# Performance work log

Hardware: AMD Instinct MI355X
Metric: run time of the kernel (lower is better)

The kernel has to match this reference:

```python
import jax, jax.numpy as jnp
import numpy as np

N, C, H, W = 16, 80, 200, 152
STRIDE = 8
PRE_NMS_THRESH = 0.2
K = 100            # pre_nms_top_n (== fpn_post_nms_top_n)
NMS_THRESH = 0.6
MIN_SIZE = 0.0


def setup_inputs() -> dict:
    key = jax.random.key(0)
    k1, k2, k3 = jax.random.split(key, 3)
    # shift logits down so only a realistic fraction passes sigmoid > 0.2
    box_cls = jax.random.normal(k1, (N, C, H, W), jnp.float32) - 2.0
    box_regression = jax.random.uniform(k2, (N, 4, H, W), jnp.float32) * 64.0
    centerness = jax.random.normal(k3, (N, 1, H, W), jnp.float32)
    ys, xs = jnp.meshgrid(jnp.arange(H), jnp.arange(W), indexing='ij')
    locations = jnp.stack([xs * STRIDE + STRIDE // 2,
                           ys * STRIDE + STRIDE // 2], axis=-1)
    locations = locations.reshape(-1, 2).astype(jnp.float32)  # [HW, 2] (x, y)
    return {"locations": locations, "box_cls": box_cls,
            "box_regression": box_regression, "centerness": centerness,
            "size_h": H * STRIDE, "size_w": W * STRIDE}


def _iou_matrix(boxes):
    # boxes: [K, 4] xyxy -> pairwise IoU [K, K]
    area = jnp.clip(boxes[:, 2] - boxes[:, 0], 0) * jnp.clip(boxes[:, 3] - boxes[:, 1], 0)
    lt = jnp.maximum(boxes[:, None, :2], boxes[None, :, :2])
    rb = jnp.minimum(boxes[:, None, 2:], boxes[None, :, 2:])
    wh = jnp.clip(rb - lt, 0)
    inter = wh[..., 0] * wh[..., 1]
    return inter / (area[:, None] + area[None, :] - inter + 1e-9)


def _nms_keep(iou, valid):
    # boxes assumed sorted by score (desc). Sequential greedy suppression.
    k = valid.shape[0]
    ar = jnp.arange(k)
    def body(i, keep):
        suppressed = jnp.any(keep & (ar < i) & (iou[i] > NMS_THRESH))
        return keep.at[i].set(valid[i] & ~suppressed)
    return jax.lax.fori_loop(0, k, body, valid)


def reference(locations, box_cls, box_regression, centerness, size_h, size_w):
    n, c = box_cls.shape[0], box_cls.shape[1]
    # N,C,H,W -> N,HW,C ; sigmoid scores
    scores = jax.nn.sigmoid(box_cls.transpose(0, 2, 3, 1).reshape(n, -1, c))
    reg = box_regression.transpose(0, 2, 3, 1).reshape(n, -1, 4)        # [n,HW,4]
    ctr = jax.nn.sigmoid(centerness.transpose(0, 2, 3, 1).reshape(n, -1))  # [n,HW]
    cand = scores > PRE_NMS_THRESH
    comb = scores * ctr[:, :, None]
    # masked flat scores; top-K == topk(per_pre_nms_top_n) with -inf padding
    masked = jnp.where(cand, comb, -jnp.inf).reshape(n, -1)
    vals, idx = jax.lax.top_k(masked, K)          # sorted desc, [n,K]
    valid = jnp.isfinite(vals)
    loc_idx = idx // c                            # flat location index in HW
    labels = idx % c + 1
    per_reg = jnp.take_along_axis(reg, loc_idx[:, :, None], axis=1)  # [n,K,4]
    per_loc = locations[loc_idx]                                     # [n,K,2]
    x1 = per_loc[..., 0] - per_reg[..., 0]
    y1 = per_loc[..., 1] - per_reg[..., 1]
    x2 = per_loc[..., 0] + per_reg[..., 2]
    y2 = per_loc[..., 1] + per_reg[..., 3]
    wmax = jnp.float32(size_w - 1)
    hmax = jnp.float32(size_h - 1)
    x1 = jnp.clip(x1, 0, wmax); x2 = jnp.clip(x2, 0, wmax)
    y1 = jnp.clip(y1, 0, hmax); y2 = jnp.clip(y2, 0, hmax)
    boxes = jnp.stack([x1, y1, x2, y2], axis=-1)  # [n,K,4]
    valid = valid & (x2 - x1 >= MIN_SIZE) & (y2 - y1 >= MIN_SIZE)
    # scores = sqrt(cls * centerness); double-where keeps grads finite
    scores_out = jnp.where(valid, jnp.sqrt(jnp.where(valid, vals, 1.0)), 0.0)
    # multi-class NMS: offset boxes per class so classes never overlap
    off = labels.astype(boxes.dtype) * jnp.float32(max(size_h, size_w))
    boxes_off = boxes + off[..., None]
    iou = jax.vmap(_iou_matrix)(boxes_off)        # [n,K,K]
    keep = jax.vmap(_nms_keep)(iou, valid)        # [n,K] bool
    scores_final = jnp.where(keep, scores_out, 0.0)
    return boxes, scores_final, labels, keep
```

## Files before the change

kernel.cpp:

```cpp
#include <hip/hip_runtime.h>
#include <math.h>

#define NIMG 16
#define NC   80
#define HH   200
#define WW   152
#define HWSZ (HH*WW)
#define HW4  (HWSZ/4)
#define KTOP 100
#define NBINS 4096
#define CAP   16384
#define FCAP  1024
#define CHUNKS4 30
#define CHUNKS 119

#define HIST_OFF 0
#define CNT_OFF  262144
#define TBIN_OFF 262208
#define CIDX_OFF 262272
#define CVAL_OFF 1310848
#define ZERO_BYTES 262272

__device__ __forceinline__ float sigf(float x){ return 1.f/(1.f+expf(-x)); }

__global__ void __launch_bounds__(256) k_hist_collect(
    const float* __restrict__ cls, const float* __restrict__ cent,
    int* __restrict__ hist, int* __restrict__ cnt,
    int* __restrict__ cand_idx, float* __restrict__ cand_val)
{
  __shared__ int lhist[NBINS];
  __shared__ int lcnt, gbase;
  __shared__ int   lidx[FCAP];
  __shared__ float lval[FCAP];
  const int n    = blockIdx.y;
  const int idx4 = blockIdx.x*256 + threadIdx.x;
  for (int b = threadIdx.x; b < NBINS; b += 256) lhist[b] = 0;
  if (threadIdx.x == 0) lcnt = 0;
  __syncthreads();
  if (idx4 < HW4) {
    const float4 ct4 = ((const float4*)cent)[n*HW4 + idx4];
    float cs[4];
    cs[0] = sigf(ct4.x); cs[1] = sigf(ct4.y); cs[2] = sigf(ct4.z); cs[3] = sigf(ct4.w);
    const float4* cp = (const float4*)(cls + (size_t)n*NC*HWSZ) + idx4;
    const int hw0 = idx4*4;
    for (int c = 0; c < NC; ++c) {
      float4 v = cp[(size_t)c*HW4];
      float x[4] = {v.x, v.y, v.z, v.w};
      #pragma unroll
      for (int e = 0; e < 4; ++e) {
        if (x[e] > -1.3867f) {
          float s = sigf(x[e]);
          if (s > 0.2f) {
            float comb = s*cs[e];
            if (comb > 0.25f) {
              int b = (int)(comb*4096.f); if (b > 4095) b = 4095;
              atomicAdd(&lhist[b], 1);
              if (comb > 0.5f) {
                int p = atomicAdd(&lcnt, 1);
                if (p < FCAP) { lidx[p] = (hw0+e)*NC + c; lval[p] = comb; }
                else {
                  int g = atomicAdd(&cnt[n], 1);
                  if (g < CAP) { cand_idx[n*CAP+g] = (hw0+e)*NC + c; cand_val[n*CAP+g] = comb; }
                }
              }
            }
          }
        }
      }
    }
  }
  __syncthreads();
  int nc = lcnt; if (nc > FCAP) nc = FCAP;
  if (threadIdx.x == 0) gbase = atomicAdd(&cnt[n], nc);
  __syncthreads();
  for (int i = threadIdx.x; i < nc; i += 256) {
    int g = gbase + i;
    if (g < CAP) { cand_idx[n*CAP+g] = lidx[i]; cand_val[n*CAP+g] = lval[i]; }
  }
  for (int b = threadIdx.x; b < NBINS; b += 256) {
    int v = lhist[b];
    if (v) atomicAdd(&hist[n*NBINS + b], v);
  }
}

__global__ void __launch_bounds__(256) k_thresh(
    const int* __restrict__ hist, int* __restrict__ tbin)
{
  __shared__ int lh[NBINS];
  __shared__ int csum[256];
  const int n = blockIdx.x, t = threadIdx.x;
  for (int b = t; b < NBINS; b += 256) lh[b] = hist[n*NBINS + b];
  __syncthreads();
  int s = 0;
  for (int b = t*16; b < t*16+16; ++b) s += lh[b];
  csum[t] = s;
  __syncthreads();
  if (t == 0) { int run = 0; for (int i = 255; i >= 0; --i) { int tmp = csum[i]; csum[i] = run; run += tmp; } }
  __syncthreads();
  int run = csum[t];
  for (int b = t*16+15; b >= t*16; --b) {
    run += lh[b];
    if (run >= KTOP && (run - lh[b]) < KTOP) tbin[n] = b;
  }
}

__global__ void __launch_bounds__(256) k_collect_fb(
    const float* __restrict__ cls, const float* __restrict__ cent,
    const int* __restrict__ tbin, int* __restrict__ cnt,
    int* __restrict__ cand_idx, float* __restrict__ cand_val)
{
  const int n = blockIdx.y;
  const int T = tbin[n];
  if (T >= 2048) return;
  __shared__ int lcnt, gbase;
  __shared__ int   lidx[FCAP];
  __shared__ float lval[FCAP];
  if (threadIdx.x == 0) lcnt = 0;
  __syncthreads();
  const int hw = blockIdx.x*256 + threadIdx.x;
  if (hw < HWSZ) {
    float csv = sigf(cent[n*HWSZ + hw]);
    const float* cp = cls + (size_t)n*NC*HWSZ + hw;
    for (int c = 0; c < NC; ++c) {
      float s = sigf(cp[(size_t)c*HWSZ]);
      if (s > 0.2f) {
        float comb = s*csv;
        if (!(comb > 0.5f)) {
          int b = (int)(comb*4096.f); if (b > 4095) b = 4095;
          if (b >= T) {
            int p = atomicAdd(&lcnt, 1);
            if (p < FCAP) { lidx[p] = hw*NC + c; lval[p] = comb; }
            else { int g = atomicAdd(&cnt[n], 1);
                   if (g < CAP) { cand_idx[n*CAP+g] = hw*NC + c; cand_val[n*CAP+g] = comb; } }
          }
        }
      }
    }
  }
  __syncthreads();
  int ncl = lcnt; if (ncl > FCAP) ncl = FCAP;
  if (threadIdx.x == 0) gbase = atomicAdd(&cnt[n], ncl);
  __syncthreads();
  for (int i = threadIdx.x; i < ncl; i += 256) {
    int g = gbase + i;
    if (g < CAP) { cand_idx[n*CAP+g] = lidx[i]; cand_val[n*CAP+g] = lval[i]; }
  }
}

__global__ void __launch_bounds__(256) k_final(
    const float* __restrict__ cls, const float* __restrict__ cent,
    const float* __restrict__ reg, const float* __restrict__ locs,
    const int* __restrict__ tbin, const int* __restrict__ cnt,
    const int* __restrict__ cand_idx, const float* __restrict__ cand_val,
    float* __restrict__ out)
{
  const int n = blockIdx.x, tid = threadIdx.x;
  __shared__ int    fidx[FCAP];
  __shared__ double fval[FCAP];
  __shared__ int fcnt;
  __shared__ int    topidx[KTOP];
  __shared__ double topval[KTOP];
  __shared__ float bx1[KTOP], by1[KTOP], bx2[KTOP], by2[KTOP], barea[KTOP];
  __shared__ float ox1[KTOP], oy1[KTOP], ox2[KTOP], oy2[KTOP], osc[KTOP];
  __shared__ int olab[KTOP];
  __shared__ unsigned char oval[KTOP], okeep[KTOP];
  if (tid == 0) fcnt = 0;
  for (int k = tid; k < KTOP; k += 256) topidx[k] = -1;
  __syncthreads();
  const int T = tbin[n];
  int m = cnt[n]; if (m > CAP) m = CAP;
  for (int i = tid; i < m; i += 256) {
    float v = cand_val[n*CAP + i];
    int b = (int)(v*4096.f); if (b > 4095) b = 4095;
    if (b >= T) { int p = atomicAdd(&fcnt, 1); if (p < FCAP) fidx[p] = cand_idx[n*CAP + i]; }
  }
  __syncthreads();
  int mf = fcnt; if (mf > FCAP) mf = FCAP;
  for (int i = tid; i < mf; i += 256) {
    int idx = fidx[i]; int loc = idx / NC; int c = idx - loc*NC;
    double s  = 1.0/(1.0 + exp(-(double)cls[(size_t)n*NC*HWSZ + (size_t)c*HWSZ + loc]));
    double ct = 1.0/(1.0 + exp(-(double)cent[n*HWSZ + loc]));
    fval[i] = s*ct;
  }
  __syncthreads();
  for (int i = tid; i < mf; i += 256) {
    double vi = fval[i]; int ii = fidx[i]; int r = 0;
    for (int j = 0; j < mf; ++j) {
      double vj = fval[j];
      r += (vj > vi) || (vj == vi && fidx[j] < ii);
    }
    if (r < KTOP) { topidx[r] = ii; topval[r] = vi; }
  }
  __syncthreads();
  if (tid < KTOP) {
    int idx = topidx[tid];
    float x1, y1, x2, y2, sc; int lab; bool vld;
    if (idx >= 0) {
      int loc = idx / NC; int c = idx - loc*NC; lab = c + 1;
      float lx = locs[2*loc], ly = locs[2*loc + 1];
      const float* rp = reg + (size_t)n*4*HWSZ;
      float dl = rp[loc], dt = rp[HWSZ + loc], dr = rp[2*HWSZ + loc], db = rp[3*HWSZ + loc];
      const float wmax = (float)(WW*8 - 1);
      const float hmax = (float)(HH*8 - 1);
      x1 = fminf(fmaxf(lx - dl, 0.f), wmax);
      x2 = fminf(fmaxf(lx + dr, 0.f), wmax);
      y1 = fminf(fmaxf(ly - dt, 0.f), hmax);
      y2 = fminf(fmaxf(ly + db, 0.f), hmax);
      vld = (x2 - x1 >= 0.f) && (y2 - y1 >= 0.f);
      sc = vld ? sqrtf((float)topval[tid]) : 0.f;
    } else { x1 = y1 = x2 = y2 = 0.f; lab = 1; vld = false; sc = 0.f; }
    ox1[tid] = x1; oy1[tid] = y1; ox2[tid] = x2; oy2[tid] = y2;
    osc[tid] = sc; olab[tid] = lab; oval[tid] = vld ? 1 : 0;
    float off = (float)lab * 1600.0f;
    float X1 = x1 + off, Y1 = y1 + off, X2 = x2 + off, Y2 = y2 + off;
    bx1[tid] = X1; by1[tid] = Y1; bx2[tid] = X2; by2[tid] = Y2;
    barea[tid] = fmaxf(X2 - X1, 0.f) * fmaxf(Y2 - Y1, 0.f);
  }
  __syncthreads();
  if (tid < 64) {
    const int lane = tid, j1 = lane + 64;
    float a_x1 = bx1[lane], a_y1 = by1[lane], a_x2 = bx2[lane], a_y2 = by2[lane], a_ar = barea[lane];
    float c_x1 = 0, c_y1 = 0, c_x2 = 0, c_y2 = 0, c_ar = 0;
    if (j1 < KTOP) { c_x1 = bx1[j1]; c_y1 = by1[j1]; c_x2 = bx2[j1]; c_y2 = by2[j1]; c_ar = barea[j1]; }
    unsigned long long k0 = 0ull, k1 = 0ull;
    for (int i = 0; i < KTOP; ++i) {
      float ix1 = bx1[i], iy1 = by1[i], ix2 = bx2[i], iy2 = by2[i], iar = barea[i];
      bool s0 = false, s1 = false;
      if (lane < i && ((k0 >> lane) & 1ull)) {
        float w = fmaxf(fminf(ix2, a_x2) - fmaxf(ix1, a_x1), 0.f);
        float h = fmaxf(fminf(iy2, a_y2) - fmaxf(iy1, a_y1), 0.f);
        float inter = w*h;
        s0 = inter / (iar + a_ar - inter + 1e-9f) > 0.6f;
      }
      if (j1 < i && ((k1 >> lane) & 1ull)) {
        float w = fmaxf(fminf(ix2, c_x2) - fmaxf(ix1, c_x1), 0.f);
        float h = fmaxf(fminf(iy2, c_y2) - fmaxf(iy1, c_y1), 0.f);
        float inter = w*h;
        s1 = inter / (iar + c_ar - inter + 1e-9f) > 0.6f;
      }
      unsigned long long b0 = __ballot(s0), b1 = __ballot(s1);
      bool keep_i = (oval[i] != 0) && ((b0 | b1) == 0ull);
      if (keep_i) { if (i < 64) k0 |= 1ull << i; else k1 |= 1ull << (i - 64); }
    }
    okeep[lane] = (unsigned char)((k0 >> lane) & 1ull);
    if (j1 < KTOP) okeep[j1] = (unsigned char)((k1 >> lane) & 1ull);
  }
  __syncthreads();
  if (tid < KTOP) {
    float* ob = out;
    float* os = out + NIMG*KTOP*4;
    float* ol = os + NIMG*KTOP;
    float* ok = ol + NIMG*KTOP;
    int base = n*KTOP + tid;
    ob[base*4 + 0] = ox1[tid]; ob[base*4 + 1] = oy1[tid];
    ob[base*4 + 2] = ox2[tid]; ob[base*4 + 3] = oy2[tid];
    bool kp = okeep[tid] != 0;
    os[base] = kp ? osc[tid] : 0.f;
    ol[base] = (float)olab[tid];
    ok[base] = kp ? 1.f : 0.f;
  }
}

extern "C" void kernel_launch(void* const* d_in, const int* in_sizes, int n_in,
                              void* d_out, int out_size, void* d_ws, size_t ws_size,
                              hipStream_t stream) {
  const float* locs = (const float*)d_in[0];
  const float* cls  = (const float*)d_in[1];
  const float* reg  = (const float*)d_in[2];
  const float* cent = (const float*)d_in[3];
  char* ws = (char*)d_ws;
  int*   hist     = (int*)(ws + HIST_OFF);
  int*   cnt      = (int*)(ws + CNT_OFF);
  int*   tbin     = (int*)(ws + TBIN_OFF);
  int*   cand_idx = (int*)(ws + CIDX_OFF);
  float* cand_val = (float*)(ws + CVAL_OFF);
  float* out = (float*)d_out;

  hipMemsetAsync(d_ws, 0, ZERO_BYTES, stream);
  dim3 gridA(CHUNKS4, NIMG);
  k_hist_collect<<<gridA, 256, 0, stream>>>(cls, cent, hist, cnt, cand_idx, cand_val);
  k_thresh<<<NIMG, 256, 0, stream>>>(hist, tbin);
  dim3 gridF(CHUNKS, NIMG);
  k_collect_fb<<<gridF, 256, 0, stream>>>(cls, cent, tbin, cnt, cand_idx, cand_val);
  k_final<<<NIMG, 256, 0, stream>>>(cls, cent, reg, locs, tbin, cnt,
                                    cand_idx, cand_val, out);
}
```

Measured before the change: 336.2 us.

## Drop global histogram pass; split class loop across blocks and refine threshold in final

```diff
diff --git a/kernel.cpp b/kernel.cpp
--- a/kernel.cpp
+++ b/kernel.cpp
@@ -10,59 +10,53 @@
 #define KTOP 100
 #define NBINS 4096
 #define CAP   16384
+#define SCAP  512
 #define FCAP  1024
+#define CPG   16
+#define CGRP  (NC/CPG)
 #define CHUNKS4 30
-#define CHUNKS 119
-
-#define HIST_OFF 0
-#define CNT_OFF  262144
-#define TBIN_OFF 262208
-#define CIDX_OFF 262272
-#define CVAL_OFF 1310848
-#define ZERO_BYTES 262272
+
+#define CNT_OFF  0
+#define TBIN_OFF 64
+#define CIDX_OFF 128
+#define CVAL_OFF (128 + NIMG*CAP*4)
+#define ZERO_BYTES 128
 
 __device__ __forceinline__ float sigf(float x){ return 1.f/(1.f+expf(-x)); }
 
-__global__ void __launch_bounds__(256) k_hist_collect(
+__global__ void __launch_bounds__(256) k_collect(
     const float* __restrict__ cls, const float* __restrict__ cent,
-    int* __restrict__ hist, int* __restrict__ cnt,
-    int* __restrict__ cand_idx, float* __restrict__ cand_val)
+    int* __restrict__ cnt, int* __restrict__ cand_idx, float* __restrict__ cand_val)
 {
-  __shared__ int lhist[NBINS];
   __shared__ int lcnt, gbase;
-  __shared__ int   lidx[FCAP];
-  __shared__ float lval[FCAP];
-  const int n    = blockIdx.y;
+  __shared__ int   lidx[SCAP];
+  __shared__ float lval[SCAP];
+  const int n = blockIdx.y, g = blockIdx.z;
   const int idx4 = blockIdx.x*256 + threadIdx.x;
-  for (int b = threadIdx.x; b < NBINS; b += 256) lhist[b] = 0;
   if (threadIdx.x == 0) lcnt = 0;
   __syncthreads();
   if (idx4 < HW4) {
     const float4 ct4 = ((const float4*)cent)[n*HW4 + idx4];
     float cs[4];
     cs[0] = sigf(ct4.x); cs[1] = sigf(ct4.y); cs[2] = sigf(ct4.z); cs[3] = sigf(ct4.w);
-    const float4* cp = (const float4*)(cls + (size_t)n*NC*HWSZ) + idx4;
+    const float4* cp = (const float4*)(cls + (size_t)n*NC*HWSZ + (size_t)g*CPG*HWSZ) + idx4;
     const int hw0 = idx4*4;
-    for (int c = 0; c < NC; ++c) {
+    #pragma unroll 4
+    for (int c = 0; c < CPG; ++c) {
       float4 v = cp[(size_t)c*HW4];
       float x[4] = {v.x, v.y, v.z, v.w};
       #pragma unroll
       for (int e = 0; e < 4; ++e) {
-        if (x[e] > -1.3867f) {
+        if (x[e] > 0.f) {
           float s = sigf(x[e]);
-          if (s > 0.2f) {
-            float comb = s*cs[e];
-            if (comb > 0.25f) {
-              int b = (int)(comb*4096.f); if (b > 4095) b = 4095;
-              atomicAdd(&lhist[b], 1);
-              if (comb > 0.5f) {
-                int p = atomicAdd(&lcnt, 1);
-                if (p < FCAP) { lidx[p] = (hw0+e)*NC + c; lval[p] = comb; }
-                else {
-                  int g = atomicAdd(&cnt[n], 1);
-                  if (g < CAP) { cand_idx[n*CAP+g] = (hw0+e)*NC + c; cand_val[n*CAP+g] = comb; }
-                }
-              }
+          float comb = s*cs[e];
+          if (comb > 0.5f) {
+            int gi = (hw0+e)*NC + (g*CPG + c);
+            int p = atomicAdd(&lcnt, 1);
+            if (p < SCAP) { lidx[p] = gi; lval[p] = comb; }
+            else {
+              int gg = atomicAdd(&cnt[n], 1);
+              if (gg < CAP) { cand_idx[n*CAP+gg] = gi; cand_val[n*CAP+gg] = comb; }
             }
           }
         }
@@ -70,80 +64,62 @@
     }
   }
   __syncthreads();
-  int nc = lcnt; if (nc > FCAP) nc = FCAP;
+  int nc = lcnt; if (nc > SCAP) nc = SCAP;
   if (threadIdx.x == 0) gbase = atomicAdd(&cnt[n], nc);
   __syncthreads();
   for (int i = threadIdx.x; i < nc; i += 256) {
-    int g = gbase + i;
-    if (g < CAP) { cand_idx[n*CAP+g] = lidx[i]; cand_val[n*CAP+g] = lval[i]; }
-  }
-  for (int b = threadIdx.x; b < NBINS; b += 256) {
-    int v = lhist[b];
-    if (v) atomicAdd(&hist[n*NBINS + b], v);
-  }
-}
-
-__global__ void __launch_bounds__(256) k_thresh(
-    const int* __restrict__ hist, int* __restrict__ tbin)
-{
-  __shared__ int lh[NBINS];
-  __shared__ int csum[256];
-  const int n = blockIdx.x, t = threadIdx.x;
-  for (int b = t; b < NBINS; b += 256) lh[b] = hist[n*NBINS + b];
-  __syncthreads();
-  int s = 0;
-  for (int b = t*16; b < t*16+16; ++b) s += lh[b];
-  csum[t] = s;
-  __syncthreads();
-  if (t == 0) { int run = 0; for (int i = 255; i >= 0; --i) { int tmp = csum[i]; csum[i] = run; run += tmp; } }
-  __syncthreads();
-  int run = csum[t];
-  for (int b = t*16+15; b >= t*16; --b) {
-    run += lh[b];
-    if (run >= KTOP && (run - lh[b]) < KTOP) tbin[n] = b;
-  }
-}
-
-__global__ void __launch_bounds__(256) k_collect_fb(
+    int g2 = gbase + i;
+    if (g2 < CAP) { cand_idx[n*CAP+g2] = lidx[i]; cand_val[n*CAP+g2] = lval[i]; }
+  }
+}
+
+__global__ void __launch_bounds__(256) k_fallback(
     const float* __restrict__ cls, const float* __restrict__ cent,
-    const int* __restrict__ tbin, int* __restrict__ cnt,
+    int* __restrict__ cnt, int* __restrict__ tbin,
     int* __restrict__ cand_idx, float* __restrict__ cand_val)
 {
-  const int n = blockIdx.y;
-  const int T = tbin[n];
-  if (T >= 2048) return;
-  __shared__ int lcnt, gbase;
-  __shared__ int   lidx[FCAP];
-  __shared__ float lval[FCAP];
-  if (threadIdx.x == 0) lcnt = 0;
-  __syncthreads();
-  const int hw = blockIdx.x*256 + threadIdx.x;
-  if (hw < HWSZ) {
-    float csv = sigf(cent[n*HWSZ + hw]);
+  const int n = blockIdx.x, tid = threadIdx.x;
+  if (cnt[n] >= KTOP) { if (tid == 0) tbin[n] = 2048; return; }
+  __shared__ int lh[NBINS];
+  __shared__ int sT;
+  for (int b = tid; b < NBINS; b += 256) lh[b] = 0;
+  __syncthreads();
+  for (int hw = tid; hw < HWSZ; hw += 256) {
+    float cs = sigf(cent[n*HWSZ + hw]);
     const float* cp = cls + (size_t)n*NC*HWSZ + hw;
     for (int c = 0; c < NC; ++c) {
       float s = sigf(cp[(size_t)c*HWSZ]);
       if (s > 0.2f) {
-        float comb = s*csv;
+        float comb = s*cs;
+        int b = (int)(comb*4096.f); if (b > 4095) b = 4095;
+        atomicAdd(&lh[b], 1);
+      }
+    }
+  }
+  __syncthreads();
+  if (tid == 0) {
+    int run = 0, T = 0;
+    for (int b = NBINS-1; b >= 0; --b) { run += lh[b]; if (run >= KTOP) { T = b; break; } }
+    sT = T; tbin[n] = T;
+  }
+  __syncthreads();
+  const int T = sT;
+  for (int hw = tid; hw < HWSZ; hw += 256) {
+    float cs = sigf(cent[n*HWSZ + hw]);
+    const float* cp = cls + (size_t)n*NC*HWSZ + hw;
+    for (int c = 0; c < NC; ++c) {
+      float s = sigf(cp[(size_t)c*HWSZ]);
+      if (s > 0.2f) {
+        float comb = s*cs;
         if (!(comb > 0.5f)) {
-          int b = (int)(comb*4096.f); if (b > 4095) b = 4095;
+          int b = (int)(comb*4096.f);
           if (b >= T) {
-            int p = atomicAdd(&lcnt, 1);
-            if (p < FCAP) { lidx[p] = hw*NC + c; lval[p] = comb; }
-            else { int g = atomicAdd(&cnt[n], 1);
-                   if (g < CAP) { cand_idx[n*CAP+g] = hw*NC + c; cand_val[n*CAP+g] = comb; } }
+            int g = atomicAdd(&cnt[n], 1);
+            if (g < CAP) { cand_idx[n*CAP+g] = hw*NC + c; cand_val[n*CAP+g] = comb; }
           }
         }
       }
     }
-  }
-  __syncthreads();
-  int ncl = lcnt; if (ncl > FCAP) ncl = FCAP;
-  if (threadIdx.x == 0) gbase = atomicAdd(&cnt[n], ncl);
-  __syncthreads();
-  for (int i = threadIdx.x; i < ncl; i += 256) {
-    int g = gbase + i;
-    if (g < CAP) { cand_idx[n*CAP+g] = lidx[i]; cand_val[n*CAP+g] = lval[i]; }
   }
 }
 
@@ -155,24 +131,47 @@
     float* __restrict__ out)
 {
   const int n = blockIdx.x, tid = threadIdx.x;
+  __shared__ int rh[256];
+  __shared__ int sR, fcnt;
   __shared__ int    fidx[FCAP];
   __shared__ double fval[FCAP];
-  __shared__ int fcnt;
   __shared__ int    topidx[KTOP];
   __shared__ double topval[KTOP];
   __shared__ float bx1[KTOP], by1[KTOP], bx2[KTOP], by2[KTOP], barea[KTOP];
   __shared__ float ox1[KTOP], oy1[KTOP], ox2[KTOP], oy2[KTOP], osc[KTOP];
   __shared__ int olab[KTOP];
   __shared__ unsigned char oval[KTOP], okeep[KTOP];
+  rh[tid] = 0;
   if (tid == 0) fcnt = 0;
   for (int k = tid; k < KTOP; k += 256) topidx[k] = -1;
   __syncthreads();
   const int T = tbin[n];
+  const float lo = (float)T * (1.f/4096.f);
+  const float scale = 256.f / (1.f - lo);
   int m = cnt[n]; if (m > CAP) m = CAP;
   for (int i = tid; i < m; i += 256) {
     float v = cand_val[n*CAP + i];
     int b = (int)(v*4096.f); if (b > 4095) b = 4095;
-    if (b >= T) { int p = atomicAdd(&fcnt, 1); if (p < FCAP) fidx[p] = cand_idx[n*CAP + i]; }
+    if (b >= T) {
+      int r = (int)((v - lo)*scale); r = r < 0 ? 0 : (r > 255 ? 255 : r);
+      atomicAdd(&rh[r], 1);
+    }
+  }
+  __syncthreads();
+  if (tid == 0) {
+    int run = 0, R = 0;
+    for (int r = 255; r >= 0; --r) { run += rh[r]; if (run >= KTOP) { R = r; break; } }
+    sR = R;
+  }
+  __syncthreads();
+  const int R = sR;
+  for (int i = tid; i < m; i += 256) {
+    float v = cand_val[n*CAP + i];
+    int b = (int)(v*4096.f); if (b > 4095) b = 4095;
+    if (b >= T) {
+      int r = (int)((v - lo)*scale); r = r < 0 ? 0 : (r > 255 ? 255 : r);
+      if (r >= R) { int p = atomicAdd(&fcnt, 1); if (p < FCAP) fidx[p] = cand_idx[n*CAP + i]; }
+    }
   }
   __syncthreads();
   int mf = fcnt; if (mf > FCAP) mf = FCAP;
@@ -269,7 +268,6 @@
   const float* reg  = (const float*)d_in[2];
   const float* cent = (const float*)d_in[3];
   char* ws = (char*)d_ws;
-  int*   hist     = (int*)(ws + HIST_OFF);
   int*   cnt      = (int*)(ws + CNT_OFF);
   int*   tbin     = (int*)(ws + TBIN_OFF);
   int*   cand_idx = (int*)(ws + CIDX_OFF);
@@ -277,11 +275,9 @@
   float* out = (float*)d_out;
 
   hipMemsetAsync(d_ws, 0, ZERO_BYTES, stream);
-  dim3 gridA(CHUNKS4, NIMG);
-  k_hist_collect<<<gridA, 256, 0, stream>>>(cls, cent, hist, cnt, cand_idx, cand_val);
-  k_thresh<<<NIMG, 256, 0, stream>>>(hist, tbin);
-  dim3 gridF(CHUNKS, NIMG);
-  k_collect_fb<<<gridF, 256, 0, stream>>>(cls, cent, tbin, cnt, cand_idx, cand_val);
+  dim3 gridC(CHUNKS4, NIMG, CGRP);
+  k_collect<<<gridC, 256, 0, stream>>>(cls, cent, cnt, cand_idx, cand_val);
+  k_fallback<<<NIMG, 256, 0, stream>>>(cls, cent, cnt, tbin, cand_idx, cand_val);
   k_final<<<NIMG, 256, 0, stream>>>(cls, cent, reg, locs, tbin, cnt,
                                     cand_idx, cand_val, out);
 }
```

Result: faster. 314.8 us (-6.4%).
